# Kernel tuning notes

Measured on AMD Instinct MI355X. Metric: run time of the kernel, lower is better.

Reference implementation:

```python
import jax, jax.numpy as jnp
import numpy as np
import math

B, S, D, H, DK, FF, L = 4, 1024, 512, 8, 64, 2048, 4
IN, NS, SD, TOPK = 768, 4, 64, 2


def _ln(x, g, b, eps=1e-5):
    mu = jnp.mean(x, -1, keepdims=True)
    var = jnp.mean((x - mu) ** 2, -1, keepdims=True)
    return (x - mu) / jnp.sqrt(var + eps) * g + b


def _pos_emb(s, d):
    pos = jnp.arange(s, dtype=jnp.float32)[:, None]
    div = jnp.exp(jnp.arange(0, d, 2, dtype=jnp.float32) * (-math.log(10000.0) / d))
    pe = jnp.zeros((s, d), jnp.float32)
    pe = pe.at[:, 0::2].set(jnp.sin(pos * div))
    pe = pe.at[:, 1::2].set(jnp.cos(pos * div))
    return pe


def setup_inputs() -> dict:
    key = jax.random.key(0)
    ks = iter(jax.random.split(key, 40))
    r = lambda *sh: jax.random.normal(next(ks), sh, jnp.float32)
    p = lambda *sh: jax.random.normal(next(ks), sh, jnp.float32) * 0.02
    inp = {
        'q_raw_seq': r(B, S, NS, IN),
        'm_seq': r(B, S, SD),
        'qa_embed': r(B, S, D),
        # MoE expert FFNs: Linear(IN,IN) -> ReLU -> Linear(IN,D)
        'exp_w1': p(NS, IN, IN), 'exp_b1': jnp.zeros((NS, IN)),
        'exp_w2': p(NS, IN, D), 'exp_b2': jnp.zeros((NS, D)),
        # router input adapter Linear(NS*IN, D)
        'adapt_w': p(NS * IN, D), 'adapt_b': jnp.zeros((D,)),
        'gate_w': p(D + SD, NS), 'gate_b': jnp.zeros((NS,)),
        'moe_ln_g': jnp.ones((D,)), 'moe_ln_b': jnp.zeros((D,)),
        # transformer blocks (kq_same=1 -> k_linear shared for q and k)
        'kw': p(L, D, D), 'kb': jnp.zeros((L, D)),
        'vw': p(L, D, D), 'vb': jnp.zeros((L, D)),
        'ow': p(L, D, D), 'ob': jnp.zeros((L, D)),
        'ln1_g': jnp.ones((L, D)), 'ln1_b': jnp.zeros((L, D)),
        'ff_w1': p(L, D, FF), 'ff_b1': jnp.zeros((L, FF)),
        'ff_w2': p(L, FF, D), 'ff_b2': jnp.zeros((L, D)),
        'ln2_g': jnp.ones((L, D)), 'ln2_b': jnp.zeros((L, D)),
    }
    return inp


def _forward(q_raw_seq, m_seq, qa_embed, exp_w1, exp_b1, exp_w2, exp_b2,
             adapt_w, adapt_b, gate_w, gate_b, moe_ln_g, moe_ln_b,
             kw, kb, vw, vb, ow, ob, ln1_g, ln1_b,
             ff_w1, ff_b1, ff_w2, ff_b2, ln2_g, ln2_b):
    # ---- PolyaParallelMoE (eval: no noise/dropout), has_stages=True ----
    h1 = jax.nn.relu(jnp.einsum('bske,kef->bskf', q_raw_seq, exp_w1) + exp_b1[None, None])
    experts = jnp.einsum('bskf,kfm->bskm', h1, exp_w2) + exp_b2[None, None]  # [B,S,4,D]
    q_flat = q_raw_seq.reshape(q_raw_seq.shape[0], q_raw_seq.shape[1], NS * IN)
    summary = jax.nn.relu(q_flat @ adapt_w + adapt_b)
    logits = jnp.concatenate([summary, m_seq], -1) @ gate_w + gate_b  # [B,S,4]
    top_vals, _ = jax.lax.top_k(logits, TOPK)
    thresh = top_vals[..., -1:]
    masked = jnp.where(logits >= thresh, logits, -jnp.inf)  # scatter top-k, -inf elsewhere
    gate_weights = jax.nn.softmax(masked, -1)
    combined = jnp.einsum('bskm,bsk->bsm', experts, gate_weights)
    q_embed = _ln(combined, moe_ln_g, moe_ln_b)

    # ---- Architecture: positional add + causal transformer blocks ----
    pe = _pos_emb(S, D)
    x = q_embed + pe
    y = qa_embed + pe
    allow = jnp.tril(jnp.ones((S, S), bool), -1)  # strict lower: np.triu(k=0)==0
    scale = 1.0 / math.sqrt(DK)
    for i in range(L):
        kh = (x @ kw[i] + kb[i]).reshape(B, S, H, DK).transpose(0, 2, 1, 3)
        vh = (y @ vw[i] + vb[i]).reshape(B, S, H, DK).transpose(0, 2, 1, 3)
        # kq_same: q = k_linear(query), query==key==x -> qh == kh
        scores = jnp.einsum('bhid,bhjd->bhij', kh, kh) * scale
        scores = jnp.where(allow, scores, -1e32)
        attn = jax.nn.softmax(scores, -1)
        attn = attn.at[:, :, 0, :].set(0.0)  # zero_pad first query row
        ctx = jnp.einsum('bhij,bhjd->bhid', attn, vh).transpose(0, 2, 1, 3).reshape(B, S, D)
        x = _ln(x + (ctx @ ow[i] + ob[i]), ln1_g[i], ln1_b[i])
        ffn = jax.nn.relu(x @ ff_w1[i] + ff_b1[i]) @ ff_w2[i] + ff_b2[i]
        x = _ln(x + ffn, ln2_g[i], ln2_b[i])
        y = x  # after first block, value stream follows torch loop (values=y fixed)
        y = qa_embed + pe  # values stay qa stream per Architecture.forward
    return x


def reference(q_raw_seq, m_seq, qa_embed, exp_w1, exp_b1, exp_w2, exp_b2,
              adapt_w, adapt_b, gate_w, gate_b, moe_ln_g, moe_ln_b,
              kw, kb, vw, vb, ow, ob, ln1_g, ln1_b,
              ff_w1, ff_b1, ff_w2, ff_b2, ln2_g, ln2_b):
    # NOTE: in Architecture.forward, each block is called with query=x, key=x, values=y
    # where y = qa_embed + pe stays fixed across blocks.
    def fwd(*a):
        return _forward(*a)
    return fwd(q_raw_seq, m_seq, qa_embed, exp_w1, exp_b1, exp_w2, exp_b2,
               adapt_w, adapt_b, gate_w, gate_b, moe_ln_g, moe_ln_b,
               kw, kb, vw, vb, ow, ob, ln1_g, ln1_b,
               ff_w1, ff_b1, ff_w2, ff_b2, ln2_g, ln2_b)
```

## Files before the change

### kernel.cpp

```cpp
#include <hip/hip_runtime.h>
#include <hip/hip_bf16.h>

typedef unsigned short u16;
typedef __attribute__((ext_vector_type(8))) short short8;
typedef __attribute__((ext_vector_type(4))) float floatx4;

template <typename T> struct is_u16 { static constexpr bool v = false; };
template <> struct is_u16<u16> { static constexpr bool v = true; };

__device__ __forceinline__ float bf2f(u16 u) {
    unsigned x = (unsigned)u << 16;
    return __uint_as_float(x);
}
__device__ __forceinline__ u16 f2bf(float f) {
    unsigned x = __float_as_uint(f);
    unsigned r = (x + 0x7fffu + ((x >> 16) & 1u)) >> 16;
    return (u16)r;
}

__device__ __forceinline__ float wave_sum(float v) {
    #pragma unroll
    for (int off = 32; off; off >>= 1) v += __shfl_xor(v, off);
    return v;
}

__device__ __forceinline__ void async16(const u16* g, const u16* lds) {
    __builtin_amdgcn_global_load_lds(
        (const __attribute__((address_space(1))) void*)g,
        (__attribute__((address_space(3))) void*)lds, 16, 0, 0);
}

__device__ __forceinline__ void load8f(const float* p, u16* dst) {
    float4 a = *(const float4*)p, b = *(const float4*)(p + 4);
    dst[0] = f2bf(a.x); dst[1] = f2bf(a.y); dst[2] = f2bf(a.z); dst[3] = f2bf(a.w);
    dst[4] = f2bf(b.x); dst[5] = f2bf(b.y); dst[6] = f2bf(b.z); dst[7] = f2bf(b.w);
}

__device__ __forceinline__ void hilo8(const float* p, u16* hi, u16* lo) {
    float4 a = *(const float4*)p, b = *(const float4*)(p + 4);
    float v[8] = {a.x, a.y, a.z, a.w, b.x, b.y, b.z, b.w};
    #pragma unroll
    for (int i = 0; i < 8; ++i) {
        u16 h = f2bf(v[i]);
        hi[i] = h;
        lo[i] = f2bf(v[i] - bf2f(h));
    }
}

__global__ __launch_bounds__(256) void hilo_conv_kernel(
    const float* __restrict__ in, u16* __restrict__ hi, u16* __restrict__ lo)
{
    const size_t i = ((size_t)blockIdx.x * 256 + threadIdx.x) * 8;
    u16 h[8], l[8];
    hilo8(in + i, h, l);
    *(uint4*)&hi[i] = *(const uint4*)h;
    *(uint4*)&lo[i] = *(const uint4*)l;
}

template <typename TA>
__device__ __forceinline__ void gemm_body(
    const TA* __restrict__ A, int lda,
    const u16* __restrict__ Bt, int ldb,
    const float* __restrict__ bias,
    float* __restrict__ Cf, u16* __restrict__ Cb, int ldc,
    int K, int act, int transC)
{
    __shared__ __align__(16) u16 Asm[128 * 32];
    __shared__ __align__(16) u16 Bsm[128 * 32];

    const int tid = threadIdx.x;
    const int lane = tid & 63;
    const int wave = tid >> 6;
    const int m0 = blockIdx.y * 128, n0 = blockIdx.x * 128;
    const int wm = (wave >> 1) * 64, wn = (wave & 1) * 64;

    const int r0 = tid >> 2;
    const int kc = (tid & 3) * 8;

    const int kq = (lane >> 4) * 8;
    const int fm = lane & 15;

    const floatx4 zz = {0.f, 0.f, 0.f, 0.f};
    floatx4 acc[4][4];
    #pragma unroll
    for (int mt = 0; mt < 4; ++mt)
        #pragma unroll
        for (int nt = 0; nt < 4; ++nt) acc[mt][nt] = zz;

    const u16* ldsA0 = Asm + wave * 512;
    const u16* ldsA1 = Asm + 2048 + wave * 512;
    const u16* ldsB0 = Bsm + wave * 512;
    const u16* ldsB1 = Bsm + 2048 + wave * 512;

    for (int kt = 0; kt < K; kt += 32) {
        if constexpr (is_u16<TA>::v) {
            async16(&A[(size_t)(m0 + r0) * lda + kt + kc],      ldsA0);
            async16(&A[(size_t)(m0 + r0 + 64) * lda + kt + kc], ldsA1);
            async16(&Bt[(size_t)(n0 + r0) * ldb + kt + kc],      ldsB0);
            async16(&Bt[(size_t)(n0 + r0 + 64) * ldb + kt + kc], ldsB1);
        } else {
            load8f(&A[(size_t)(m0 + r0) * lda + kt + kc],      &Asm[r0 * 32 + kc]);
            load8f(&A[(size_t)(m0 + r0 + 64) * lda + kt + kc], &Asm[(r0 + 64) * 32 + kc]);
            *(uint4*)&Bsm[r0 * 32 + kc]        = *(const uint4*)&Bt[(size_t)(n0 + r0) * ldb + kt + kc];
            *(uint4*)&Bsm[(r0 + 64) * 32 + kc] = *(const uint4*)&Bt[(size_t)(n0 + r0 + 64) * ldb + kt + kc];
        }
        __syncthreads();

        short8 af[4], bfr[4];
        #pragma unroll
        for (int mt = 0; mt < 4; ++mt)
            af[mt] = *(const short8*)&Asm[(wm + mt * 16 + fm) * 32 + kq];
        #pragma unroll
        for (int nt = 0; nt < 4; ++nt)
            bfr[nt] = *(const short8*)&Bsm[(wn + nt * 16 + fm) * 32 + kq];

        #pragma unroll
        for (int mt = 0; mt < 4; ++mt)
            #pragma unroll
            for (int nt = 0; nt < 4; ++nt)
                acc[mt][nt] = __builtin_amdgcn_mfma_f32_16x16x32_bf16(
                    af[mt], bfr[nt], acc[mt][nt], 0, 0, 0);
        __syncthreads();
    }

    const int cr = (lane >> 4) * 4;
    #pragma unroll
    for (int mt = 0; mt < 4; ++mt) {
        #pragma unroll
        for (int nt = 0; nt < 4; ++nt) {
            const int col = n0 + wn + nt * 16 + fm;
            const float bz = bias ? bias[col] : 0.f;
            #pragma unroll
            for (int r = 0; r < 4; ++r) {
                const int row = m0 + wm + mt * 16 + cr + r;
                float v = acc[mt][nt][r] + bz;
                if (act) v = fmaxf(v, 0.f);
                if (Cf) Cf[(size_t)row * ldc + col] = v;
                if (Cb) {
                    if (transC)
                        Cb[(((size_t)(row >> 10) * 512 + col) << 10) + (row & 1023)] = f2bf(v);
                    else
                        Cb[(size_t)row * ldc + col] = f2bf(v);
                }
            }
        }
    }
}

template <typename TA>
__global__ __launch_bounds__(256) void gemm_bf16(
    const TA* __restrict__ A, int lda, long strideAz,
    const u16* __restrict__ Bt, int ldb, long strideBz,
    const float* __restrict__ bias, int strideBiasZ,
    float* __restrict__ Cf, u16* __restrict__ Cb, int ldc, long strideCz,
    int K, int act, int transC)
{
    A += (size_t)blockIdx.z * strideAz;
    Bt += (size_t)blockIdx.z * strideBz;
    if (bias) bias += (size_t)blockIdx.z * strideBiasZ;
    if (Cf) Cf += (size_t)blockIdx.z * strideCz;
    if (Cb) Cb += (size_t)blockIdx.z * strideCz;
    gemm_body<TA>(A, lda, Bt, ldb, bias, Cf, Cb, ldc, K, act, transC);
}

__global__ __launch_bounds__(256) void gemm_kv(
    const u16* __restrict__ xb, const u16* __restrict__ yb,
    const u16* __restrict__ kwt, const u16* __restrict__ vwt,
    const float* __restrict__ kb, const float* __restrict__ vb,
    u16* __restrict__ khb, u16* __restrict__ vhT)
{
    if (blockIdx.z == 0)
        gemm_body<u16>(xb, 512, kwt, 512, kb, nullptr, khb, 512, 512, 0, 0);
    else
        gemm_body<u16>(yb, 512, vwt, 512, vb, nullptr, vhT, 512, 512, 0, 1);
}

__global__ __launch_bounds__(256) void gemm_f32split(
    const u16* __restrict__ Ah, const u16* __restrict__ Al, int lda,
    const u16* __restrict__ Bh, const u16* __restrict__ Bl, int ldb,
    float* __restrict__ Cf, int ldc, long strideCz,
    int kz)
{
    __shared__ __align__(16) u16 Ahs[128 * 32];
    __shared__ __align__(16) u16 Als[128 * 32];
    __shared__ __align__(16) u16 Bhs[128 * 32];
    __shared__ __align__(16) u16 Bls[128 * 32];

    const int tid = threadIdx.x;
    const int lane = tid & 63;
    const int wave = tid >> 6;
    const int m0 = blockIdx.y * 128, n0 = blockIdx.x * 128;
    const int wm = (wave >> 1) * 64, wn = (wave & 1) * 64;
    const int k0 = blockIdx.z * kz;
    Cf += (size_t)blockIdx.z * strideCz;

    const int r0 = tid >> 2;
    const int kc = (tid & 3) * 8;
    const int kq = (lane >> 4) * 8;
    const int fm = lane & 15;

    const floatx4 zz = {0.f, 0.f, 0.f, 0.f};
    floatx4 acc[4][4];
    #pragma unroll
    for (int mt = 0; mt < 4; ++mt)
        #pragma unroll
        for (int nt = 0; nt < 4; ++nt) acc[mt][nt] = zz;

    const u16* ldsAh0 = Ahs + wave * 512;
    const u16* ldsAh1 = Ahs + 2048 + wave * 512;
    const u16* ldsAl0 = Als + wave * 512;
    const u16* ldsAl1 = Als + 2048 + wave * 512;
    const u16* ldsBh0 = Bhs + wave * 512;
    const u16* ldsBh1 = Bhs + 2048 + wave * 512;
    const u16* ldsBl0 = Bls + wave * 512;
    const u16* ldsBl1 = Bls + 2048 + wave * 512;

    for (int kt = 0; kt < kz; kt += 32) {
        const size_t ka = (size_t)(m0 + r0) * lda + k0 + kt + kc;
        const size_t kb = (size_t)(n0 + r0) * ldb + k0 + kt + kc;
        async16(&Ah[ka],                     ldsAh0);
        async16(&Ah[ka + (size_t)64 * lda],  ldsAh1);
        async16(&Al[ka],                     ldsAl0);
        async16(&Al[ka + (size_t)64 * lda],  ldsAl1);
        async16(&Bh[kb],                     ldsBh0);
        async16(&Bh[kb + (size_t)64 * ldb],  ldsBh1);
        async16(&Bl[kb],                     ldsBl0);
        async16(&Bl[kb + (size_t)64 * ldb],  ldsBl1);
        __syncthreads();

        short8 ah[4], al[4], bh[4], bl[4];
        #pragma unroll
        for (int mt = 0; mt < 4; ++mt) {
            ah[mt] = *(const short8*)&Ahs[(wm + mt * 16 + fm) * 32 + kq];
            al[mt] = *(const short8*)&Als[(wm + mt * 16 + fm) * 32 + kq];
        }
        #pragma unroll
        for (int nt = 0; nt < 4; ++nt) {
            bh[nt] = *(const short8*)&Bhs[(wn + nt * 16 + fm) * 32 + kq];
            bl[nt] = *(const short8*)&Bls[(wn + nt * 16 + fm) * 32 + kq];
        }

        #pragma unroll
        for (int mt = 0; mt < 4; ++mt)
            #pragma unroll
            for (int nt = 0; nt < 4; ++nt) {
                acc[mt][nt] = __builtin_amdgcn_mfma_f32_16x16x32_bf16(
                    ah[mt], bh[nt], acc[mt][nt], 0, 0, 0);
                acc[mt][nt] = __builtin_amdgcn_mfma_f32_16x16x32_bf16(
                    al[mt], bh[nt], acc[mt][nt], 0, 0, 0);
                acc[mt][nt] = __builtin_amdgcn_mfma_f32_16x16x32_bf16(
                    ah[mt], bl[nt], acc[mt][nt], 0, 0, 0);
            }
        __syncthreads();
    }

    const int cr = (lane >> 4) * 4;
    #pragma unroll
    for (int mt = 0; mt < 4; ++mt) {
        #pragma unroll
        for (int nt = 0; nt < 4; ++nt) {
            const int col = n0 + wn + nt * 16 + fm;
            #pragma unroll
            for (int r = 0; r < 4; ++r) {
                const int row = m0 + wm + mt * 16 + cr + r;
                Cf[(size_t)row * ldc + col] = acc[mt][nt][r];
            }
        }
    }
}

__global__ __launch_bounds__(64) void gate_fused_kernel(
    const float* __restrict__ ps, const float* __restrict__ adapt_b,
    const float* __restrict__ m_seq,
    const float* __restrict__ gw, const float* __restrict__ gb,
    float* __restrict__ gates)
{
    const int r = blockIdx.x, t = threadIdx.x;
    float p0 = 0.f, p1 = 0.f, p2 = 0.f, p3 = 0.f;
    const float* pr = ps + (size_t)r * 512;
    for (int j = t; j < 512; j += 64) {
        float v = pr[j] + pr[j + 2097152] + pr[j + 4194304] + pr[j + 6291456] + adapt_b[j];
        float s = fmaxf(v, 0.f);
        const float* g = gw + (size_t)j * 4;
        p0 += s * g[0]; p1 += s * g[1]; p2 += s * g[2]; p3 += s * g[3];
    }
    {
        float m = m_seq[(size_t)r * 64 + t];
        const float* g = gw + (size_t)(512 + t) * 4;
        p0 += m * g[0]; p1 += m * g[1]; p2 += m * g[2]; p3 += m * g[3];
    }
    p0 = wave_sum(p0); p1 = wave_sum(p1); p2 = wave_sum(p2); p3 = wave_sum(p3);
    if (t == 0) {
        float lg[4] = { p0 + gb[0], p1 + gb[1], p2 + gb[2], p3 + gb[3] };
        float m1 = -INFINITY, m2 = -INFINITY;
        #pragma unroll
        for (int k = 0; k < 4; ++k) {
            float v = lg[k];
            if (v > m1) { m2 = m1; m1 = v; }
            else if (v > m2) { m2 = v; }
        }
        float wv[4], s = 0.f;
        #pragma unroll
        for (int k = 0; k < 4; ++k) {
            wv[k] = (lg[k] >= m2) ? __expf(lg[k] - m1) : 0.f;
            s += wv[k];
        }
        float inv = 1.f / s;
        #pragma unroll
        for (int k = 0; k < 4; ++k) gates[(size_t)r * 4 + k] = wv[k] * inv;
    }
}

__global__ __launch_bounds__(256) void tconv_kernel(
    const float* __restrict__ in, u16* __restrict__ out, int K, int N)
{
    __shared__ float t[32][33];
    const int n0 = blockIdx.x * 32, k0 = blockIdx.y * 32;
    const size_t bo = (size_t)blockIdx.z * K * N;
    const int tx = threadIdx.x & 31, ty = threadIdx.x >> 5;
    const float* src = in + bo;
    u16* dst = out + bo;
    #pragma unroll
    for (int r = ty; r < 32; r += 8) t[r][tx] = src[(size_t)(k0 + r) * N + n0 + tx];
    __syncthreads();
    #pragma unroll
    for (int r = ty; r < 32; r += 8) dst[(size_t)(n0 + r) * K + k0 + tx] = f2bf(t[tx][r]);
}

__global__ __launch_bounds__(256) void tconv_hilo_kernel(
    const float* __restrict__ in, u16* __restrict__ outh, u16* __restrict__ outl,
    int K, int N)
{
    __shared__ float t[32][33];
    const int n0 = blockIdx.x * 32, k0 = blockIdx.y * 32;
    const int tx = threadIdx.x & 31, ty = threadIdx.x >> 5;
    #pragma unroll
    for (int r = ty; r < 32; r += 8) t[r][tx] = in[(size_t)(k0 + r) * N + n0 + tx];
    __syncthreads();
    #pragma unroll
    for (int r = ty; r < 32; r += 8) {
        float v = t[tx][r];
        u16 h = f2bf(v);
        outh[(size_t)(n0 + r) * K + k0 + tx] = h;
        outl[(size_t)(n0 + r) * K + k0 + tx] = f2bf(v - bf2f(h));
    }
}

__global__ void pe_kernel(float* __restrict__ pe)
{
    int idx = blockIdx.x * 256 + threadIdx.x;
    int s = idx >> 9, d = idx & 511;
    float div = expf((float)(d & ~1) * (-9.210340371976184f / 512.0f));
    float ang = (float)s * div;
    pe[idx] = (d & 1) ? cosf(ang) : sinf(ang);
}

__global__ void y_kernel(const float* __restrict__ qa, const float* __restrict__ pe,
                         u16* __restrict__ yb)
{
    int idx = blockIdx.x * 256 + threadIdx.x;
    yb[idx] = f2bf(qa[idx] + pe[idx & 524287]);
}

__global__ __launch_bounds__(64) void moe_ln_kernel(
    const u16* __restrict__ experts, const float* __restrict__ gates,
    const float* __restrict__ g, const float* __restrict__ bb,
    const float* __restrict__ pe, float* __restrict__ x, u16* __restrict__ xb)
{
    const int r = blockIdx.x, t = threadIdx.x;
    const u16* e = experts + (size_t)r * 2048;
    const float g0 = gates[r * 4 + 0], g1 = gates[r * 4 + 1];
    const float g2 = gates[r * 4 + 2], g3 = gates[r * 4 + 3];
    float v[8];
    #pragma unroll
    for (int it = 0; it < 8; ++it) {
        int d = t + it * 64;
        v[it] = g0 * bf2f(e[d]) + g1 * bf2f(e[512 + d])
              + g2 * bf2f(e[1024 + d]) + g3 * bf2f(e[1536 + d]);
    }
    float s = 0.f;
    #pragma unroll
    for (int it = 0; it < 8; ++it) s += v[it];
    s = wave_sum(s);
    const float mu = s * (1.f / 512.f);
    float q = 0.f;
    #pragma unroll
    for (int it = 0; it < 8; ++it) { float dd = v[it] - mu; q += dd * dd; }
    q = wave_sum(q);
    const float rstd = rsqrtf(q * (1.f / 512.f) + 1e-5f);
    const float* per = pe + (size_t)(r & 1023) * 512;
    #pragma unroll
    for (int it = 0; it < 8; ++it) {
        int d = t + it * 64;
        float o = (v[it] - mu) * rstd * g[d] + bb[d] + per[d];
        x[(size_t)r * 512 + d] = o;
        xb[(size_t)r * 512 + d] = f2bf(o);
    }
}

__global__ __launch_bounds__(64) void add_ln_kernel(
    float* __restrict__ x, u16* __restrict__ xb,
    const float* __restrict__ t0, const float* __restrict__ t1,
    const float* __restrict__ bias,
    const float* __restrict__ g, const float* __restrict__ bb,
    float* __restrict__ out2)
{
    const int r = blockIdx.x, t = threadIdx.x;
    float* xr = x + (size_t)r * 512;
    float v[8];
    #pragma unroll
    for (int it = 0; it < 8; ++it) {
        int d = t + it * 64;
        float tv = t0[(size_t)r * 512 + d];
        if (t1) tv += t1[(size_t)r * 512 + d];
        if (bias) tv += bias[d];
        v[it] = xr[d] + tv;
    }
    float s = 0.f;
    #pragma unroll
    for (int it = 0; it < 8; ++it) s += v[it];
    s = wave_sum(s);
    const float mu = s * (1.f / 512.f);
    float q = 0.f;
    #pragma unroll
    for (int it = 0; it < 8; ++it) { float dd = v[it] - mu; q += dd * dd; }
    q = wave_sum(q);
    const float rstd = rsqrtf(q * (1.f / 512.f) + 1e-5f);
    #pragma unroll
    for (int it = 0; it < 8; ++it) {
        int d = t + it * 64;
        float o = (v[it] - mu) * rstd * g[d] + bb[d];
        xr[d] = o;
        xb[(size_t)r * 512 + d] = f2bf(o);
        if (out2) out2[(size_t)r * 512 + d] = o;
    }
}

__global__ __launch_bounds__(256) void attn_kernel(
    const u16* __restrict__ kh, const u16* __restrict__ vhT,
    u16* __restrict__ ctx)
{
    __shared__ __align__(16) u16 Qs[64 * 64];
    __shared__ __align__(16) u16 Ks[64 * 64];
    __shared__ __align__(16) u16 Vt[64 * 72];
    __shared__ __align__(16) u16 Ps[64 * 72];

    const int tid = threadIdx.x;
    const int lane = tid & 63, wave = tid >> 6;
    const int quad = lane >> 4, fm = lane & 15;
    const int b = blockIdx.x, h = blockIdx.y;
    const int bz = blockIdx.z;
    const int it = (bz < 8) ? bz : (23 - bz);

    const u16* khb = kh + ((size_t)b * 1024) * 512 + h * 64;
    const u16* vtb = vhT + ((size_t)(b * 512 + h * 64)) * 1024;

    const int lj = tid >> 2;
    const int lc = tid & 3;

    {
        const u16* src = khb + (size_t)(it * 64 + lj) * 512 + lc * 16;
        *(uint4*)&Qs[lj * 64 + lc * 16]     = *(const uint4*)src;
        *(uint4*)&Qs[lj * 64 + lc * 16 + 8] = *(const uint4*)(src + 8);
    }

    const floatx4 zz = {0.f, 0.f, 0.f, 0.f};
    floatx4 o_acc[4];
    #pragma unroll
    for (int nt = 0; nt < 4; ++nt) o_acc[nt] = zz;
    float m_run[4] = { -INFINITY, -INFINITY, -INFINITY, -INFINITY };
    float l_run[4] = {};

    __syncthreads();

    for (int jt = 0; jt <= it; ++jt) {
        {
            const u16* ksrc = khb + (size_t)(jt * 64 + lj) * 512 + lc * 16;
            *(uint4*)&Ks[lj * 64 + lc * 16]     = *(const uint4*)ksrc;
            *(uint4*)&Ks[lj * 64 + lc * 16 + 8] = *(const uint4*)(ksrc + 8);
            const u16* vsrc = vtb + (size_t)lj * 1024 + jt * 64 + lc * 16;
            *(uint4*)&Vt[lj * 72 + lc * 16]     = *(const uint4*)vsrc;
            *(uint4*)&Vt[lj * 72 + lc * 16 + 8] = *(const uint4*)(vsrc + 8);
        }
        __syncthreads();

        floatx4 s_acc[4];
        #pragma unroll
        for (int nt = 0; nt < 4; ++nt) s_acc[nt] = zz;
        #pragma unroll
        for (int ks = 0; ks < 2; ++ks) {
            short8 af = *(const short8*)&Qs[(wave * 16 + fm) * 64 + ks * 32 + quad * 8];
            #pragma unroll
            for (int nt = 0; nt < 4; ++nt) {
                short8 bf = *(const short8*)&Ks[(nt * 16 + fm) * 64 + ks * 32 + quad * 8];
                s_acc[nt] = __builtin_amdgcn_mfma_f32_16x16x32_bf16(af, bf, s_acc[nt], 0, 0, 0);
            }
        }

        const bool diag = (jt == it);
        #pragma unroll
        for (int r = 0; r < 4; ++r) {
            const int rowi = wave * 16 + quad * 4 + r;
            float sv[4];
            #pragma unroll
            for (int nt = 0; nt < 4; ++nt) {
                float s = s_acc[nt][r] * 0.125f;
                if (diag && (nt * 16 + fm) >= rowi) s = -INFINITY;
                sv[nt] = s;
            }
            float mx = fmaxf(fmaxf(sv[0], sv[1]), fmaxf(sv[2], sv[3]));
            #pragma unroll
            for (int off = 1; off < 16; off <<= 1) mx = fmaxf(mx, __shfl_xor(mx, off));
            const float mn = fmaxf(m_run[r], mx);
            const float mfix = (mn == -INFINITY) ? 0.f : mn;
            const float alpha = (m_run[r] == -INFINITY) ? 0.f : __expf(m_run[r] - mn);
            m_run[r] = mn;
            float rs = 0.f;
            #pragma unroll
            for (int nt = 0; nt < 4; ++nt) {
                float p = __expf(sv[nt] - mfix);
                Ps[rowi * 72 + nt * 16 + fm] = f2bf(p);
                rs += p;
            }
            #pragma unroll
            for (int off = 1; off < 16; off <<= 1) rs += __shfl_xor(rs, off);
            l_run[r] = l_run[r] * alpha + rs;
            #pragma unroll
            for (int nt = 0; nt < 4; ++nt) o_acc[nt][r] *= alpha;
        }
        __syncthreads();

        #pragma unroll
        for (int ks = 0; ks < 2; ++ks) {
            short8 af = *(const short8*)&Ps[(wave * 16 + fm) * 72 + ks * 32 + quad * 8];
            #pragma unroll
            for (int nt = 0; nt < 4; ++nt) {
                short8 bf = *(const short8*)&Vt[(nt * 16 + fm) * 72 + ks * 32 + quad * 8];
                o_acc[nt] = __builtin_amdgcn_mfma_f32_16x16x32_bf16(af, bf, o_acc[nt], 0, 0, 0);
            }
        }
        __syncthreads();
    }

    u16* cb = ctx + ((size_t)b * 1024 + (size_t)it * 64 + wave * 16) * 512 + h * 64;
    #pragma unroll
    for (int r = 0; r < 4; ++r) {
        const int row = quad * 4 + r;
        const float inv = (l_run[r] > 0.f) ? 1.f / l_run[r] : 0.f;
        #pragma unroll
        for (int nt = 0; nt < 4; ++nt)
            cb[(size_t)row * 512 + nt * 16 + fm] = f2bf(o_acc[nt][r] * inv);
    }
}

extern "C" void kernel_launch(void* const* d_in, const int* in_sizes, int n_in,
                              void* d_out, int out_size, void* d_ws, size_t ws_size,
                              hipStream_t stream)
{
    const float* q_raw   = (const float*)d_in[0];
    const float* m_seq   = (const float*)d_in[1];
    const float* qa      = (const float*)d_in[2];
    const float* exp_w1  = (const float*)d_in[3];
    const float* exp_b1  = (const float*)d_in[4];
    const float* exp_w2  = (const float*)d_in[5];
    const float* exp_b2  = (const float*)d_in[6];
    const float* adapt_w = (const float*)d_in[7];
    const float* adapt_b = (const float*)d_in[8];
    const float* gate_w  = (const float*)d_in[9];
    const float* gate_b  = (const float*)d_in[10];
    const float* moe_g   = (const float*)d_in[11];
    const float* moe_b   = (const float*)d_in[12];
    const float* kw      = (const float*)d_in[13];
    const float* kb      = (const float*)d_in[14];
    const float* vw      = (const float*)d_in[15];
    const float* vb      = (const float*)d_in[16];
    const float* ow      = (const float*)d_in[17];
    const float* ob      = (const float*)d_in[18];
    const float* ln1g    = (const float*)d_in[19];
    const float* ln1b    = (const float*)d_in[20];
    const float* fw1     = (const float*)d_in[21];
    const float* fb1     = (const float*)d_in[22];
    const float* fw2     = (const float*)d_in[23];
    const float* fb2     = (const float*)d_in[24];
    const float* ln2g    = (const float*)d_in[25];
    const float* ln2b    = (const float*)d_in[26];
    float* out = (float*)d_out;

    const size_t NEED = 125829120ull;
    if (ws_size < NEED) return;

    char* base = (char*)d_ws;
    float* x  = (float*)(base + 0);
    u16*  xb  = (u16*)(base + 8388608);
    u16*  yb  = (u16*)(base + 12582912);
    char* G = base + 16777216;
    u16*   w1t     = (u16*)(G + 0);
    u16*   w2t     = (u16*)(G + 4718592);
    float* psum    = (float*)(G + 7864320);
    u16*   h1b4    = (u16*)(G + 7864320);
    u16*   expb    = (u16*)(G + 33030144);
    float* pe      = (float*)(G + 49807360);
    float* gates   = (float*)(G + 51904512);
    u16*   adwh    = (u16*)(G + 52428800);
    u16*   adwl    = (u16*)(G + 55574528);
    u16*   qhi     = (u16*)(G + 58720256);
    u16*   qlo     = (u16*)(G + 83886080);
    u16*   kwt  = (u16*)(G + 0);
    u16*   vwt  = (u16*)(G + 2097152);
    u16*   owt  = (u16*)(G + 4194304);
    u16*   fw1t = (u16*)(G + 6291456);
    u16*   fw2t = (u16*)(G + 14680064);
    u16*   khb  = (u16*)(G + 23068672);
    u16*   vhT  = (u16*)(G + 27262976);
    u16*   ctxb = (u16*)(G + 31457280);
    float* p    = (float*)(G + 35651584);
    u16*   ffhb = (u16*)(G + 44040192);
    float* ps0  = (float*)(G + 23068672);

    pe_kernel<<<2048, 256, 0, stream>>>(pe);
    hilo_conv_kernel<<<6144, 256, 0, stream>>>(q_raw, qhi, qlo);
    tconv_kernel<<<dim3(24, 24, 4), 256, 0, stream>>>(exp_w1, w1t, 768, 768);
    tconv_kernel<<<dim3(16, 24, 4), 256, 0, stream>>>(exp_w2, w2t, 768, 512);
    tconv_hilo_kernel<<<dim3(16, 96), 256, 0, stream>>>(adapt_w, adwh, adwl, 3072, 512);

    gemm_f32split<<<dim3(4, 32, 4), 256, 0, stream>>>(
        qhi, qlo, 3072, adwh, adwl, 3072, psum, 512, 2097152L, 768);
    gate_fused_kernel<<<4096, 64, 0, stream>>>(
        psum, adapt_b, m_seq, gate_w, gate_b, gates);

    gemm_bf16<u16><<<dim3(6, 32, 4), 256, 0, stream>>>(
        qhi, 3072, 768L, w1t, 768, 589824L, exp_b1, 768,
        nullptr, h1b4, 768, 3145728L, 768, 1, 0);
    gemm_bf16<u16><<<dim3(4, 32, 4), 256, 0, stream>>>(
        h1b4, 768, 3145728L, w2t, 768, 393216L, exp_b2, 512,
        nullptr, expb, 2048, 512L, 768, 0, 0);
    moe_ln_kernel<<<4096, 64, 0, stream>>>(expb, gates, moe_g, moe_b, pe, x, xb);
    y_kernel<<<8192, 256, 0, stream>>>(qa, pe, yb);

    tconv_kernel<<<dim3(16, 16, 4), 256, 0, stream>>>(kw, kwt, 512, 512);
    tconv_kernel<<<dim3(16, 16, 4), 256, 0, stream>>>(vw, vwt, 512, 512);
    tconv_kernel<<<dim3(16, 16, 4), 256, 0, stream>>>(ow, owt, 512, 512);
    tconv_kernel<<<dim3(64, 16, 4), 256, 0, stream>>>(fw1, fw1t, 512, 2048);
    tconv_kernel<<<dim3(16, 64, 4), 256, 0, stream>>>(fw2, fw2t, 2048, 512);

    for (int i = 0; i < 4; ++i) {
        gemm_kv<<<dim3(4, 32, 2), 256, 0, stream>>>(
            xb, yb, kwt + (size_t)i * 262144, vwt + (size_t)i * 262144,
            kb + i * 512, vb + i * 512, khb, vhT);
        attn_kernel<<<dim3(4, 8, 16), 256, 0, stream>>>(khb, vhT, ctxb);
        gemm_bf16<u16><<<dim3(4, 32), 256, 0, stream>>>(
            ctxb, 512, 0L, owt + (size_t)i * 262144, 512, 0L, ob + i * 512, 0,
            p, nullptr, 512, 0L, 512, 0, 0);
        add_ln_kernel<<<4096, 64, 0, stream>>>(
            x, xb, p, nullptr, nullptr, ln1g + i * 512, ln1b + i * 512, nullptr);
        gemm_bf16<u16><<<dim3(16, 32), 256, 0, stream>>>(
            xb, 512, 0L, fw1t + (size_t)i * 1048576, 512, 0L, fb1 + i * 2048, 0,
            nullptr, ffhb, 2048, 0L, 512, 1, 0);
        gemm_bf16<u16><<<dim3(4, 32, 2), 256, 0, stream>>>(
            ffhb, 2048, 1024L, fw2t + (size_t)i * 1048576, 2048, 1024L, nullptr, 0,
            ps0, nullptr, 512, 2097152L, 1024, 0, 0);
        add_ln_kernel<<<4096, 64, 0, stream>>>(
            x, xb, ps0, ps0 + 2097152, fb2 + i * 512,
            ln2g + i * 512, ln2b + i * 512, (i == 3) ? out : nullptr);
    }
}
```

Before: 954.1 us.

## Double GEMM K-step to 64, fuse y into moe_ln, merge weight transposes

The bf16 GEMM body now stages two 32-wide K slices per iteration, which halves the number of barrier pairs per K and doubles the MFMA work between syncs at the cost of twice the shared memory per block. The y = qa + pe conversion is folded into the MoE layernorm kernel, dropping one kernel launch and one reread of pe. The three 512x512 weight transposes are merged into a single launch. Larger LDS use could reduce occupancy.

```diff
diff --git a/kernel.cpp b/kernel.cpp
--- a/kernel.cpp
+++ b/kernel.cpp
@@ -65,8 +65,8 @@
     float* __restrict__ Cf, u16* __restrict__ Cb, int ldc,
     int K, int act, int transC)
 {
-    __shared__ __align__(16) u16 Asm[128 * 32];
-    __shared__ __align__(16) u16 Bsm[128 * 32];
+    __shared__ __align__(16) u16 Asm[2 * 128 * 32];
+    __shared__ __align__(16) u16 Bsm[2 * 128 * 32];
 
     const int tid = threadIdx.x;
     const int lane = tid & 63;
@@ -87,39 +87,46 @@
         #pragma unroll
         for (int nt = 0; nt < 4; ++nt) acc[mt][nt] = zz;
 
-    const u16* ldsA0 = Asm + wave * 512;
-    const u16* ldsA1 = Asm + 2048 + wave * 512;
-    const u16* ldsB0 = Bsm + wave * 512;
-    const u16* ldsB1 = Bsm + 2048 + wave * 512;
-
-    for (int kt = 0; kt < K; kt += 32) {
+    const u16* ldsA = Asm + wave * 512;
+    const u16* ldsB = Bsm + wave * 512;
+
+    for (int kt = 0; kt < K; kt += 64) {
         if constexpr (is_u16<TA>::v) {
-            async16(&A[(size_t)(m0 + r0) * lda + kt + kc],      ldsA0);
-            async16(&A[(size_t)(m0 + r0 + 64) * lda + kt + kc], ldsA1);
-            async16(&Bt[(size_t)(n0 + r0) * ldb + kt + kc],      ldsB0);
-            async16(&Bt[(size_t)(n0 + r0 + 64) * ldb + kt + kc], ldsB1);
+            #pragma unroll
+            for (int h = 0; h < 2; ++h) {
+                async16(&A[(size_t)(m0 + r0) * lda + kt + h * 32 + kc],      ldsA + h * 4096);
+                async16(&A[(size_t)(m0 + r0 + 64) * lda + kt + h * 32 + kc], ldsA + h * 4096 + 2048);
+                async16(&Bt[(size_t)(n0 + r0) * ldb + kt + h * 32 + kc],      ldsB + h * 4096);
+                async16(&Bt[(size_t)(n0 + r0 + 64) * ldb + kt + h * 32 + kc], ldsB + h * 4096 + 2048);
+            }
         } else {
-            load8f(&A[(size_t)(m0 + r0) * lda + kt + kc],      &Asm[r0 * 32 + kc]);
-            load8f(&A[(size_t)(m0 + r0 + 64) * lda + kt + kc], &Asm[(r0 + 64) * 32 + kc]);
-            *(uint4*)&Bsm[r0 * 32 + kc]        = *(const uint4*)&Bt[(size_t)(n0 + r0) * ldb + kt + kc];
-            *(uint4*)&Bsm[(r0 + 64) * 32 + kc] = *(const uint4*)&Bt[(size_t)(n0 + r0 + 64) * ldb + kt + kc];
+            #pragma unroll
+            for (int h = 0; h < 2; ++h) {
+                load8f(&A[(size_t)(m0 + r0) * lda + kt + h * 32 + kc],      &Asm[h * 4096 + r0 * 32 + kc]);
+                load8f(&A[(size_t)(m0 + r0 + 64) * lda + kt + h * 32 + kc], &Asm[h * 4096 + (r0 + 64) * 32 + kc]);
+                *(uint4*)&Bsm[h * 4096 + r0 * 32 + kc]        = *(const uint4*)&Bt[(size_t)(n0 + r0) * ldb + kt + h * 32 + kc];
+                *(uint4*)&Bsm[h * 4096 + (r0 + 64) * 32 + kc] = *(const uint4*)&Bt[(size_t)(n0 + r0 + 64) * ldb + kt + h * 32 + kc];
+            }
         }
         __syncthreads();
 
-        short8 af[4], bfr[4];
-        #pragma unroll
-        for (int mt = 0; mt < 4; ++mt)
-            af[mt] = *(const short8*)&Asm[(wm + mt * 16 + fm) * 32 + kq];
-        #pragma unroll
-        for (int nt = 0; nt < 4; ++nt)
-            bfr[nt] = *(const short8*)&Bsm[(wn + nt * 16 + fm) * 32 + kq];
-
-        #pragma unroll
-        for (int mt = 0; mt < 4; ++mt)
+        #pragma unroll
+        for (int h = 0; h < 2; ++h) {
+            short8 af[4], bfr[4];
+            #pragma unroll
+            for (int mt = 0; mt < 4; ++mt)
+                af[mt] = *(const short8*)&Asm[h * 4096 + (wm + mt * 16 + fm) * 32 + kq];
             #pragma unroll
             for (int nt = 0; nt < 4; ++nt)
-                acc[mt][nt] = __builtin_amdgcn_mfma_f32_16x16x32_bf16(
-                    af[mt], bfr[nt], acc[mt][nt], 0, 0, 0);
+                bfr[nt] = *(const short8*)&Bsm[h * 4096 + (wn + nt * 16 + fm) * 32 + kq];
+
+            #pragma unroll
+            for (int mt = 0; mt < 4; ++mt)
+                #pragma unroll
+                for (int nt = 0; nt < 4; ++nt)
+                    acc[mt][nt] = __builtin_amdgcn_mfma_f32_16x16x32_bf16(
+                        af[mt], bfr[nt], acc[mt][nt], 0, 0, 0);
+        }
         __syncthreads();
     }
 
@@ -327,6 +334,27 @@
     for (int r = ty; r < 32; r += 8) dst[(size_t)(n0 + r) * K + k0 + tx] = f2bf(t[tx][r]);
 }
 
+__global__ __launch_bounds__(256) void tconv3_kernel(
+    const float* __restrict__ kw, const float* __restrict__ vw, const float* __restrict__ ow,
+    u16* __restrict__ kwt, u16* __restrict__ vwt, u16* __restrict__ owt)
+{
+    __shared__ float t[32][33];
+    const int z = blockIdx.z;
+    const int sel = z >> 2, li = z & 3;
+    const float* in = (sel == 0) ? kw : (sel == 1) ? vw : ow;
+    u16* outp = (sel == 0) ? kwt : (sel == 1) ? vwt : owt;
+    const size_t bo = (size_t)li * 262144;
+    const int n0 = blockIdx.x * 32, k0 = blockIdx.y * 32;
+    const int tx = threadIdx.x & 31, ty = threadIdx.x >> 5;
+    const float* src = in + bo;
+    u16* dst = outp + bo;
+    #pragma unroll
+    for (int r = ty; r < 32; r += 8) t[r][tx] = src[(size_t)(k0 + r) * 512 + n0 + tx];
+    __syncthreads();
+    #pragma unroll
+    for (int r = ty; r < 32; r += 8) dst[(size_t)(n0 + r) * 512 + k0 + tx] = f2bf(t[tx][r]);
+}
+
 __global__ __launch_bounds__(256) void tconv_hilo_kernel(
     const float* __restrict__ in, u16* __restrict__ outh, u16* __restrict__ outl,
     int K, int N)
@@ -355,17 +383,11 @@
     pe[idx] = (d & 1) ? cosf(ang) : sinf(ang);
 }
 
-__global__ void y_kernel(const float* __restrict__ qa, const float* __restrict__ pe,
-                         u16* __restrict__ yb)
-{
-    int idx = blockIdx.x * 256 + threadIdx.x;
-    yb[idx] = f2bf(qa[idx] + pe[idx & 524287]);
-}
-
 __global__ __launch_bounds__(64) void moe_ln_kernel(
     const u16* __restrict__ experts, const float* __restrict__ gates,
     const float* __restrict__ g, const float* __restrict__ bb,
-    const float* __restrict__ pe, float* __restrict__ x, u16* __restrict__ xb)
+    const float* __restrict__ pe, const float* __restrict__ qa,
+    float* __restrict__ x, u16* __restrict__ xb, u16* __restrict__ yb)
 {
     const int r = blockIdx.x, t = threadIdx.x;
     const u16* e = experts + (size_t)r * 2048;
@@ -392,9 +414,11 @@
     #pragma unroll
     for (int it = 0; it < 8; ++it) {
         int d = t + it * 64;
-        float o = (v[it] - mu) * rstd * g[d] + bb[d] + per[d];
+        float pv = per[d];
+        float o = (v[it] - mu) * rstd * g[d] + bb[d] + pv;
         x[(size_t)r * 512 + d] = o;
         xb[(size_t)r * 512 + d] = f2bf(o);
+        yb[(size_t)r * 512 + d] = f2bf(qa[(size_t)r * 512 + d] + pv);
     }
 }
 
@@ -634,12 +658,9 @@
     gemm_bf16<u16><<<dim3(4, 32, 4), 256, 0, stream>>>(
         h1b4, 768, 3145728L, w2t, 768, 393216L, exp_b2, 512,
         nullptr, expb, 2048, 512L, 768, 0, 0);
-    moe_ln_kernel<<<4096, 64, 0, stream>>>(expb, gates, moe_g, moe_b, pe, x, xb);
-    y_kernel<<<8192, 256, 0, stream>>>(qa, pe, yb);
-
-    tconv_kernel<<<dim3(16, 16, 4), 256, 0, stream>>>(kw, kwt, 512, 512);
-    tconv_kernel<<<dim3(16, 16, 4), 256, 0, stream>>>(vw, vwt, 512, 512);
-    tconv_kernel<<<dim3(16, 16, 4), 256, 0, stream>>>(ow, owt, 512, 512);
+    moe_ln_kernel<<<4096, 64, 0, stream>>>(expb, gates, moe_g, moe_b, pe, qa, x, xb, yb);
+
+    tconv3_kernel<<<dim3(16, 16, 12), 256, 0, stream>>>(kw, vw, ow, kwt, vwt, owt);
     tconv_kernel<<<dim3(64, 16, 4), 256, 0, stream>>>(fw1, fw1t, 512, 2048);
     tconv_kernel<<<dim3(16, 64, 4), 256, 0, stream>>>(fw2, fw2t, 2048, 512);
 
```

New measurement: 925.8 us. 3.0% less time.
